# Kernel optimization log

Hardware: AMD Instinct MI355X
Metric: run time of the kernel (lower is better)

Reference implementation:

```python
import jax, jax.numpy as jnp
import numpy as np

B, M, E, K = 2048, 768, 16384, 32
EPS = 1e-8  # torch F.cosine_similarity default eps


def setup_inputs() -> dict:
    key = jax.random.key(0)
    ks = jax.random.split(key, 13)
    s_m = 1.0 / np.sqrt(M)  # nn.Linear(M, E) init bound
    s_e = 1.0 / np.sqrt(E)  # nn.Linear(E, M) init bound
    u = lambda k, shape, s: jax.random.uniform(k, shape, jnp.float32, -s, s)
    return {
        "x": jax.random.normal(ks[0], (B, M), jnp.float32),
        "enc_w": u(ks[1], (E, M), s_m), "enc_b": u(ks[2], (E,), s_m),
        "dec_w": u(ks[3], (M, E), s_e), "dec_b": u(ks[4], (M,), s_e),
        "enc1_w": u(ks[5], (E, M), s_m), "enc1_b": u(ks[6], (E,), s_m),
        "dec1_w": u(ks[7], (M, E), s_e), "dec1_b": u(ks[8], (M,), s_e),
        "enc2_w": u(ks[9], (E, M), s_m), "enc2_b": u(ks[10], (E,), s_m),
        "dec2_w": u(ks[11], (M, E), s_e), "dec2_b": u(ks[12], (M,), s_e),
        "k": K,
    }


def _aux_loss(a_BE, win_BE, c1_BE, c2_BE, dp_ME, d1_ME, d2_ME):
    # Faithful reduction of the B x M x E cosine-similarity along M:
    #   scaled_parent[b,:,e] = dp[:,e]*a[b,e];  scaled_child uses d1/d2 per winner mask.
    # cos_sim needs only M-dim dot products / norms of decoder columns.
    np2_E = jnp.sum(dp_ME * dp_ME, axis=0)   # ||dp_e||^2
    n1_E = jnp.sum(d1_ME * d1_ME, axis=0)
    n2_E = jnp.sum(d2_ME * d2_ME, axis=0)
    dp1_E = jnp.sum(dp_ME * d1_ME, axis=0)   # <dp_e, d1_e>
    dp2_E = jnp.sum(dp_ME * d2_ME, axis=0)
    c_BE = jnp.where(win_BE, c1_BE, c2_BE)
    dpc_BE = jnp.where(win_BE, dp1_E, dp2_E)
    nc_BE = jnp.where(win_BE, n1_E, n2_E)
    a2 = a_BE * a_BE
    dot = a2 * np2_E + a_BE * c_BE * dpc_BE                      # <parent, parent+child>
    norm_p = jnp.abs(a_BE) * jnp.sqrt(np2_E)                     # ||parent||
    comb2 = a2 * np2_E + 2.0 * a_BE * c_BE * dpc_BE + c_BE * c_BE * nc_BE
    norm_c = jnp.sqrt(jnp.maximum(comb2, 0.0))                   # ||parent+child||
    cos = dot / (jnp.maximum(norm_p, EPS) * jnp.maximum(norm_c, EPS))
    active = a_BE > 0
    return -jnp.sum(jnp.where(active, cos, 0.0)) / a_BE.shape[0]


def reference(x, enc_w, enc_b, dec_w, dec_b, enc1_w, enc1_b, dec1_w, dec1_b,
              enc2_w, enc2_b, dec2_w, dec2_b, k):
    Bn = x.shape[0]
    En = enc_w.shape[0]
    pre_BE = x @ enc_w.T + enc_b
    vals, idx = jax.lax.top_k(pre_BE, k)                         # [B,k]
    sae_BE = jnp.zeros_like(pre_BE).at[jnp.arange(Bn)[:, None], idx].set(vals)
    num_live_parent = jnp.zeros((En,), bool).at[idx.ravel()].set(True).sum()

    pre1_BE = x @ enc1_w.T + enc1_b
    pre2_BE = x @ enc2_w.T + enc2_b
    active = sae_BE != 0.0
    m1_BE = jnp.where(active, pre1_BE, 0.0)
    m2_BE = jnp.where(active, pre2_BE, 0.0)
    win_BE = m1_BE > m2_BE
    f1_BE = jnp.where(win_BE, m1_BE, 0.0)
    f2_BE = jnp.where(~win_BE, m2_BE, 0.0)
    num_live_c1 = jnp.any(f1_BE != 0, axis=0).sum()
    num_live_c2 = jnp.any(f2_BE != 0, axis=0).sum()

    recon_BM = (sae_BE @ dec_w.T + dec_b) + (f1_BE @ dec1_w.T + dec1_b) + (f2_BE @ dec2_w.T + dec2_b)

    sg = jax.lax.stop_gradient
    aux = _aux_loss(sg(sae_BE), sg(win_BE), sg(f1_BE), sg(f2_BE), dec_w, dec1_w, dec2_w)
    return recon_BM, (num_live_parent, num_live_c1, num_live_c2), aux
```

## Files before the change

### kernel.cpp

```cpp
#include <hip/hip_runtime.h>
#include <cstdint>
#include <cstddef>

#define B_N 2048
#define M_N 768
#define E_N 16384
#define K_N 32
#define EPSF 1e-8f

typedef __attribute__((ext_vector_type(8))) short short8;
typedef __attribute__((ext_vector_type(4))) float floatx4;
typedef __attribute__((ext_vector_type(4))) unsigned short ushort4v;

__device__ inline unsigned short f2bf(float f) {
  unsigned int u = __float_as_uint(f);
  unsigned int r = (u + 0x7fffu + ((u >> 16) & 1u)) >> 16;
  return (unsigned short)r;
}
__device__ inline float bf2f(unsigned short h) {
  return __uint_as_float(((unsigned int)h) << 16);
}

__global__ __launch_bounds__(256) void split_kernel(const float* __restrict__ in,
                                                    unsigned short* __restrict__ hi,
                                                    unsigned short* __restrict__ lo,
                                                    int n4) {
  int i = blockIdx.x * 256 + threadIdx.x;
  if (i >= n4) return;
  float4 v = ((const float4*)in)[i];
  ushort4v h, l;
  h.x = f2bf(v.x); l.x = f2bf(v.x - bf2f(h.x));
  h.y = f2bf(v.y); l.y = f2bf(v.y - bf2f(h.y));
  h.z = f2bf(v.z); l.z = f2bf(v.z - bf2f(h.z));
  h.w = f2bf(v.w); l.w = f2bf(v.w - bf2f(h.w));
  ((ushort4v*)hi)[i] = h;
  ((ushort4v*)lo)[i] = l;
}

__global__ void prep_dec_kernel(const float* __restrict__ dw, const float* __restrict__ d1,
                                const float* __restrict__ d2,
                                float* __restrict__ dT0, float* __restrict__ dT1,
                                float* __restrict__ dT2, float* __restrict__ stats) {
  __shared__ float t0[32][33], t1[32][33], t2[32][33];
  __shared__ float ps[5][8][32];
  int tx = threadIdx.x;
  int ty = threadIdx.y;
  int e = blockIdx.x * 32 + tx;
  float s0 = 0.f, s1 = 0.f, s2 = 0.f, s3 = 0.f, s4 = 0.f;
  for (int r = 0; r < 32; r += 8) {
    int m = blockIdx.y * 32 + ty + r;
    float a  = dw[(size_t)m * E_N + e];
    float b1 = d1[(size_t)m * E_N + e];
    float b2 = d2[(size_t)m * E_N + e];
    t0[ty + r][tx] = a;
    t1[ty + r][tx] = b1;
    t2[ty + r][tx] = b2;
    s0 = fmaf(a, a, s0);
    s1 = fmaf(b1, b1, s1);
    s2 = fmaf(b2, b2, s2);
    s3 = fmaf(a, b1, s3);
    s4 = fmaf(a, b2, s4);
  }
  ps[0][ty][tx] = s0; ps[1][ty][tx] = s1; ps[2][ty][tx] = s2;
  ps[3][ty][tx] = s3; ps[4][ty][tx] = s4;
  __syncthreads();
  int m2 = blockIdx.y * 32 + tx;
  for (int r = 0; r < 32; r += 8) {
    int e2 = blockIdx.x * 32 + ty + r;
    dT0[(size_t)e2 * M_N + m2] = t0[tx][ty + r];
    dT1[(size_t)e2 * M_N + m2] = t1[tx][ty + r];
    dT2[(size_t)e2 * M_N + m2] = t2[tx][ty + r];
  }
  if (ty == 0) {
    float a0 = 0.f, a1 = 0.f, a2 = 0.f, a3 = 0.f, a4 = 0.f;
#pragma unroll
    for (int q = 0; q < 8; ++q) {
      a0 += ps[0][q][tx]; a1 += ps[1][q][tx]; a2 += ps[2][q][tx];
      a3 += ps[3][q][tx]; a4 += ps[4][q][tx];
    }
    atomicAdd(&stats[e], a0);
    atomicAdd(&stats[E_N + e], a1);
    atomicAdd(&stats[2 * E_N + e], a2);
    atomicAdd(&stats[3 * E_N + e], a3);
    atomicAdd(&stats[4 * E_N + e], a4);
  }
}

#define TM 128
#define TN 128
#define TK 32
#define LDK 40

__global__ __launch_bounds__(256) void gemm_mfma_kernel(
    const unsigned short* __restrict__ Ahi, const unsigned short* __restrict__ Alo,
    const unsigned short* __restrict__ Bhi, const unsigned short* __restrict__ Blo,
    const float* __restrict__ bias, float* __restrict__ C) {
  __shared__ __align__(16) unsigned short As_hi[TM * LDK];
  __shared__ __align__(16) unsigned short As_lo[TM * LDK];
  __shared__ __align__(16) unsigned short Bs_hi[TM * LDK];
  __shared__ __align__(16) unsigned short Bs_lo[TM * LDK];

  int tid = threadIdx.x;
  int lane = tid & 63;
  int wave = tid >> 6;
  int i0 = blockIdx.y * TM;
  int j0 = blockIdx.x * TN;
  int wm = (wave >> 1) * 64;
  int wn = (wave & 1) * 64;

  int row0 = tid >> 2, c40 = tid & 3;
  int row1 = 64 + (tid >> 2), c41 = tid & 3;
  const unsigned short* pAhi0 = Ahi + (size_t)(i0 + row0) * M_N + c40 * 8;
  const unsigned short* pAhi1 = Ahi + (size_t)(i0 + row1) * M_N + c41 * 8;
  const unsigned short* pAlo0 = Alo + (size_t)(i0 + row0) * M_N + c40 * 8;
  const unsigned short* pAlo1 = Alo + (size_t)(i0 + row1) * M_N + c41 * 8;
  const unsigned short* pBhi0 = Bhi + (size_t)(j0 + row0) * M_N + c40 * 8;
  const unsigned short* pBhi1 = Bhi + (size_t)(j0 + row1) * M_N + c41 * 8;
  const unsigned short* pBlo0 = Blo + (size_t)(j0 + row0) * M_N + c40 * 8;
  const unsigned short* pBlo1 = Blo + (size_t)(j0 + row1) * M_N + c41 * 8;
  int l0 = row0 * LDK + c40 * 8;
  int l1 = row1 * LDK + c41 * 8;

  floatx4 acc[4][4];
#pragma unroll
  for (int i = 0; i < 4; ++i)
#pragma unroll
    for (int j = 0; j < 4; ++j) acc[i][j] = (floatx4){0.f, 0.f, 0.f, 0.f};

  int fr = lane & 15;
  int fk = (lane >> 4) * 8;

  short8 vAh0 = *(const short8*)pAhi0;
  short8 vAh1 = *(const short8*)pAhi1;
  short8 vAl0 = *(const short8*)pAlo0;
  short8 vAl1 = *(const short8*)pAlo1;
  short8 vBh0 = *(const short8*)pBhi0;
  short8 vBh1 = *(const short8*)pBhi1;
  short8 vBl0 = *(const short8*)pBlo0;
  short8 vBl1 = *(const short8*)pBlo1;

  for (int k0 = 0; k0 < M_N; k0 += TK) {
    __syncthreads();
    *(short8*)&As_hi[l0] = vAh0;
    *(short8*)&As_hi[l1] = vAh1;
    *(short8*)&As_lo[l0] = vAl0;
    *(short8*)&As_lo[l1] = vAl1;
    *(short8*)&Bs_hi[l0] = vBh0;
    *(short8*)&Bs_hi[l1] = vBh1;
    *(short8*)&Bs_lo[l0] = vBl0;
    *(short8*)&Bs_lo[l1] = vBl1;
    __syncthreads();

    if (k0 + TK < M_N) {
      int d = k0 + TK;
      vAh0 = *(const short8*)(pAhi0 + d);
      vAh1 = *(const short8*)(pAhi1 + d);
      vAl0 = *(const short8*)(pAlo0 + d);
      vAl1 = *(const short8*)(pAlo1 + d);
      vBh0 = *(const short8*)(pBhi0 + d);
      vBh1 = *(const short8*)(pBhi1 + d);
      vBl0 = *(const short8*)(pBlo0 + d);
      vBl1 = *(const short8*)(pBlo1 + d);
    }

    short8 ah[4], al[4], bh[4], bl[4];
#pragma unroll
    for (int t = 0; t < 4; ++t) {
      int ar = (wm + t * 16 + fr) * LDK + fk;
      int br = (wn + t * 16 + fr) * LDK + fk;
      ah[t] = *(const short8*)&As_hi[ar];
      al[t] = *(const short8*)&As_lo[ar];
      bh[t] = *(const short8*)&Bs_hi[br];
      bl[t] = *(const short8*)&Bs_lo[br];
    }
#pragma unroll
    for (int mi = 0; mi < 4; ++mi)
#pragma unroll
      for (int ni = 0; ni < 4; ++ni) {
        acc[mi][ni] = __builtin_amdgcn_mfma_f32_16x16x32_bf16(ah[mi], bh[ni], acc[mi][ni], 0, 0, 0);
        acc[mi][ni] = __builtin_amdgcn_mfma_f32_16x16x32_bf16(ah[mi], bl[ni], acc[mi][ni], 0, 0, 0);
        acc[mi][ni] = __builtin_amdgcn_mfma_f32_16x16x32_bf16(al[mi], bh[ni], acc[mi][ni], 0, 0, 0);
      }
  }

#pragma unroll
  for (int mi = 0; mi < 4; ++mi) {
    int rbase = i0 + wm + mi * 16 + (lane >> 4) * 4;
#pragma unroll
    for (int ni = 0; ni < 4; ++ni) {
      int col = j0 + wn + ni * 16 + (lane & 15);
      float bb = bias[col];
#pragma unroll
      for (int r = 0; r < 4; ++r) {
        C[(size_t)(rbase + r) * E_N + col] = acc[mi][ni][r] + bb;
      }
    }
  }
}

__global__ __launch_bounds__(256) void topk_kernel(const float* __restrict__ pre,
                                                   int* __restrict__ topk_idx,
                                                   float* __restrict__ topk_val,
                                                   int* __restrict__ live_p) {
  int b = blockIdx.x;
  int tid = threadIdx.x;
  const float* row = pre + (size_t)b * E_N;

  __shared__ unsigned int hist[2048];
  __shared__ float candV[2048];
  __shared__ int candI[2048];
  __shared__ float defV[K_N];
  __shared__ int defI[K_N];
  __shared__ int s_T, s_nDef, s_nCand;

  for (int i = tid; i < 2048; i += 256) hist[i] = 0;
  if (tid == 0) { s_nDef = 0; s_nCand = 0; }
  __syncthreads();

  for (int j = 0; j < E_N / 1024; ++j) {
    float4 v = ((const float4*)row)[tid + j * 256];
    float f[4] = {v.x, v.y, v.z, v.w};
#pragma unroll
    for (int q = 0; q < 4; ++q) {
      unsigned int u = __float_as_uint(f[q]);
      unsigned int key = (u & 0x80000000u) ? ~u : (u | 0x80000000u);
      atomicAdd(&hist[key >> 21], 1u);
    }
  }
  __syncthreads();

  if (tid == 0) {
    unsigned int cum = 0;
    for (int bk = 2047; bk >= 0; --bk) {
      cum += hist[bk];
      if (cum >= K_N) { s_T = bk; break; }
    }
  }
  __syncthreads();
  int T = s_T;

  for (int j = 0; j < E_N / 1024; ++j) {
    int i4 = tid + j * 256;
    float4 v = ((const float4*)row)[i4];
    float f[4] = {v.x, v.y, v.z, v.w};
#pragma unroll
    for (int q = 0; q < 4; ++q) {
      float vv = f[q];
      unsigned int u = __float_as_uint(vv);
      unsigned int key = (u & 0x80000000u) ? ~u : (u | 0x80000000u);
      int bk = key >> 21;
      if (bk > T) {
        int d = atomicAdd(&s_nDef, 1);
        defV[d] = vv;
        defI[d] = i4 * 4 + q;
      } else if (bk == T) {
        int c = atomicAdd(&s_nCand, 1);
        candV[c] = vv;
        candI[c] = i4 * 4 + q;
      }
    }
  }
  __syncthreads();
  int nDef = s_nDef;
  int nCand = s_nCand;
  int need = K_N - nDef;

  if (tid < nDef) {
    topk_idx[b * K_N + tid] = defI[tid];
    topk_val[b * K_N + tid] = defV[tid];
    live_p[defI[tid]] = 1;
  }
  for (int c = tid; c < nCand; c += 256) {
    float v = candV[c];
    int idx = candI[c];
    int r = 0;
    for (int j2 = 0; j2 < nCand; ++j2) {
      float vj = candV[j2];
      r += (vj > v) || (vj == v && candI[j2] < idx);
    }
    if (r < need) {
      int slot = nDef + r;
      topk_idx[b * K_N + slot] = idx;
      topk_val[b * K_N + slot] = v;
      live_p[idx] = 1;
    }
  }
}

__global__ __launch_bounds__(256) void child_recon_kernel(
    const float* __restrict__ x, const float* __restrict__ e1w, const float* __restrict__ e1b,
    const float* __restrict__ e2w, const float* __restrict__ e2b,
    const int* __restrict__ topk_idx, const float* __restrict__ topk_val,
    int* __restrict__ live_c1, int* __restrict__ live_c2,
    const float* __restrict__ stats, float* __restrict__ aux_sum,
    const float* __restrict__ decT0, const float* __restrict__ decT1,
    const float* __restrict__ decT2,
    const float* __restrict__ db0, const float* __restrict__ db1,
    const float* __restrict__ db2, float* __restrict__ out) {
  int b = blockIdx.x;
  int tid = threadIdx.x;
  int lane = tid & 63;
  int wave = tid >> 6;

  __shared__ float xs[M_N];
  __shared__ int es[K_N];
  __shared__ float as[K_N], cs[K_N];
  __shared__ int wf[K_N];
  __shared__ float wsum[4];

  if (tid < K_N) {
    es[tid] = topk_idx[b * K_N + tid];
    as[tid] = topk_val[b * K_N + tid];
  }
  for (int i = tid; i < M_N; i += 256) xs[i] = x[(size_t)b * M_N + i];
  __syncthreads();

  float cos_acc = 0.f;
  for (int s = wave; s < K_N; s += 4) {
    int e = es[s];
    float a = as[s];
    if (a != 0.f) {
      float d1 = 0.f, d2 = 0.f;
#pragma unroll
      for (int j = 0; j < 3; ++j) {
        int m = (lane << 2) + j * 256;
        float4 xv = *(const float4*)&xs[m];
        float4 w1 = *(const float4*)&e1w[(size_t)e * M_N + m];
        float4 w2 = *(const float4*)&e2w[(size_t)e * M_N + m];
        d1 += xv.x * w1.x + xv.y * w1.y + xv.z * w1.z + xv.w * w1.w;
        d2 += xv.x * w2.x + xv.y * w2.y + xv.z * w2.z + xv.w * w2.w;
      }
#pragma unroll
      for (int off = 32; off > 0; off >>= 1) {
        d1 += __shfl_down(d1, off);
        d2 += __shfl_down(d2, off);
      }
      if (lane == 0) {
        float m1 = d1 + e1b[e];
        float m2 = d2 + e2b[e];
        bool win = m1 > m2;
        float f1 = win ? m1 : 0.f;
        float f2 = win ? 0.f : m2;
        float c = win ? f1 : f2;
        cs[s] = c;
        wf[s] = win ? 1 : 0;
        if (f1 != 0.f) live_c1[e] = 1;
        if (f2 != 0.f) live_c2[e] = 1;
        if (a > 0.f) {
          float np2e = stats[e];
          float nce = win ? stats[E_N + e] : stats[2 * E_N + e];
          float dpc = win ? stats[3 * E_N + e] : stats[4 * E_N + e];
          float a2 = a * a;
          float dot = a2 * np2e + a * c * dpc;
          float normp = fabsf(a) * sqrtf(np2e);
          float comb2 = a2 * np2e + 2.f * a * c * dpc + c * c * nce;
          float normc = sqrtf(fmaxf(comb2, 0.f));
          cos_acc += dot / (fmaxf(normp, EPSF) * fmaxf(normc, EPSF));
        }
      }
    } else if (lane == 0) {
      cs[s] = 0.f;
      wf[s] = 0;
    }
  }
  if (lane == 0) wsum[wave] = cos_acc;
  __syncthreads();
  if (tid == 0) atomicAdd(aux_sum, wsum[0] + wsum[1] + wsum[2] + wsum[3]);

  float acc0 = db0[tid] + db1[tid] + db2[tid];
  float acc1 = db0[tid + 256] + db1[tid + 256] + db2[tid + 256];
  float acc2 = db0[tid + 512] + db1[tid + 512] + db2[tid + 512];

  for (int s = 0; s < K_N; ++s) {
    float a = as[s];
    float c = cs[s];
    if (a == 0.f && c == 0.f) continue;
    int e = es[s];
    const float* col = decT0 + (size_t)e * M_N;
    acc0 = fmaf(a, col[tid], acc0);
    acc1 = fmaf(a, col[tid + 256], acc1);
    acc2 = fmaf(a, col[tid + 512], acc2);
    if (c != 0.f) {
      const float* ccol = (wf[s] ? decT1 : decT2) + (size_t)e * M_N;
      acc0 = fmaf(c, ccol[tid], acc0);
      acc1 = fmaf(c, ccol[tid + 256], acc1);
      acc2 = fmaf(c, ccol[tid + 512], acc2);
    }
  }
  out[(size_t)b * M_N + tid] = acc0;
  out[(size_t)b * M_N + tid + 256] = acc1;
  out[(size_t)b * M_N + tid + 512] = acc2;
}

__global__ void finalize_kernel(const int* __restrict__ live_p, const int* __restrict__ live_c1,
                                const int* __restrict__ live_c2, const float* __restrict__ aux_sum,
                                float* __restrict__ out_tail) {
  int tid = threadIdx.x;
  int c0 = 0, c1 = 0, c2 = 0;
  for (int i = tid; i < E_N; i += 256) {
    c0 += live_p[i];
    c1 += live_c1[i];
    c2 += live_c2[i];
  }
  __shared__ int r0[256], r1[256], r2[256];
  r0[tid] = c0; r1[tid] = c1; r2[tid] = c2;
  __syncthreads();
  for (int s = 128; s > 0; s >>= 1) {
    if (tid < s) { r0[tid] += r0[tid + s]; r1[tid] += r1[tid + s]; r2[tid] += r2[tid + s]; }
    __syncthreads();
  }
  if (tid == 0) {
    out_tail[0] = (float)r0[0];
    out_tail[1] = (float)r1[0];
    out_tail[2] = (float)r2[0];
    out_tail[3] = -aux_sum[0] / (float)B_N;
  }
}

extern "C" void kernel_launch(void* const* d_in, const int* in_sizes, int n_in,
                              void* d_out, int out_size, void* d_ws, size_t ws_size,
                              hipStream_t stream) {
  const float* x     = (const float*)d_in[0];
  const float* enc_w = (const float*)d_in[1];
  const float* enc_b = (const float*)d_in[2];
  const float* dec_w = (const float*)d_in[3];
  const float* dec_b = (const float*)d_in[4];
  const float* e1w   = (const float*)d_in[5];
  const float* e1b   = (const float*)d_in[6];
  const float* d1w   = (const float*)d_in[7];
  const float* d1b   = (const float*)d_in[8];
  const float* e2w   = (const float*)d_in[9];
  const float* e2b   = (const float*)d_in[10];
  const float* d2w   = (const float*)d_in[11];
  const float* d2b   = (const float*)d_in[12];

  float* wsf = (float*)d_ws;

  const size_t PRE_F = (size_t)B_N * E_N;
  const size_t XSP_F = (size_t)B_N * M_N / 2;
  const size_t ESP_F = (size_t)E_N * M_N / 2;
  const size_t DEC_F = (size_t)E_N * M_N;
  const size_t BIG_F = PRE_F + 2 * XSP_F + 2 * ESP_F;

  float* pre = wsf;
  unsigned short* xhi  = (unsigned short*)(wsf + PRE_F);
  unsigned short* xlo  = (unsigned short*)(wsf + PRE_F + XSP_F);
  unsigned short* ewhi = (unsigned short*)(wsf + PRE_F + 2 * XSP_F);
  unsigned short* ewlo = (unsigned short*)(wsf + PRE_F + 2 * XSP_F + ESP_F);
  float* decT0 = wsf;
  float* decT1 = wsf + DEC_F;
  float* decT2 = wsf + 2 * DEC_F;

  size_t off = BIG_F;
  float* stats  = wsf + off;
  int*   livep  = (int*)(wsf + off + 5 * (size_t)E_N);
  int*   livec1 = livep + E_N;
  int*   livec2 = livep + 2 * E_N;
  float* auxs   = (float*)(livep + 3 * E_N);
  off += 8 * (size_t)E_N + 64;
  off &= ~(size_t)63;
  int*   tidx = (int*)(wsf + off);    off += (size_t)B_N * K_N;
  float* tval = wsf + off;            off += (size_t)B_N * K_N;

  hipMemsetAsync(stats, 0, (8 * (size_t)E_N + 1) * sizeof(float), stream);

  split_kernel<<<(B_N * M_N / 4 + 255) / 256, 256, 0, stream>>>(x, xhi, xlo, B_N * M_N / 4);
  split_kernel<<<(E_N * M_N / 4 + 255) / 256, 256, 0, stream>>>(enc_w, ewhi, ewlo, E_N * M_N / 4);

  gemm_mfma_kernel<<<dim3(E_N / TN, B_N / TM), 256, 0, stream>>>(xhi, xlo, ewhi, ewlo, enc_b, pre);

  topk_kernel<<<B_N, 256, 0, stream>>>(pre, tidx, tval, livep);

  prep_dec_kernel<<<dim3(E_N / 32, M_N / 32), dim3(32, 8), 0, stream>>>(
      dec_w, d1w, d2w, decT0, decT1, decT2, stats);

  float* out = (float*)d_out;
  child_recon_kernel<<<B_N, 256, 0, stream>>>(x, e1w, e1b, e2w, e2b, tidx, tval,
                                              livec1, livec2, stats, auxs,
                                              decT0, decT1, decT2, dec_b, d1b, d2b, out);

  finalize_kernel<<<1, 256, 0, stream>>>(livep, livec1, livec2, auxs,
                                         out + (size_t)B_N * M_N);
}
```

Before: 691.0 us.

## Merge split kernels, parallelize top-k threshold scan, split encoder GEMM in halves

Merges the two bf16 hi/lo split launches into one kernel. In top-k, the shared histogram becomes four per-wave copies to reduce atomic contention, and the serial single-thread threshold search is replaced by a block-wide suffix scan. The encoder GEMM is launched as two half-batch kernels on the same stream. That split gives no overlap by itself and adds a launch, while the extra histogram copies increase LDS use.

```diff
diff --git a/kernel.cpp b/kernel.cpp
--- a/kernel.cpp
+++ b/kernel.cpp
@@ -21,20 +21,31 @@
   return __uint_as_float(((unsigned int)h) << 16);
 }
 
-__global__ __launch_bounds__(256) void split_kernel(const float* __restrict__ in,
-                                                    unsigned short* __restrict__ hi,
-                                                    unsigned short* __restrict__ lo,
-                                                    int n4) {
+__global__ __launch_bounds__(256) void split2_kernel(
+    const float* __restrict__ inA, unsigned short* __restrict__ hiA,
+    unsigned short* __restrict__ loA, int n4A,
+    const float* __restrict__ inB, unsigned short* __restrict__ hiB,
+    unsigned short* __restrict__ loB, int n4B) {
   int i = blockIdx.x * 256 + threadIdx.x;
-  if (i >= n4) return;
-  float4 v = ((const float4*)in)[i];
+  const float* in;
+  unsigned short* hi;
+  unsigned short* lo;
+  int idx;
+  if (i < n4A) {
+    in = inA; hi = hiA; lo = loA; idx = i;
+  } else {
+    idx = i - n4A;
+    if (idx >= n4B) return;
+    in = inB; hi = hiB; lo = loB;
+  }
+  float4 v = ((const float4*)in)[idx];
   ushort4v h, l;
   h.x = f2bf(v.x); l.x = f2bf(v.x - bf2f(h.x));
   h.y = f2bf(v.y); l.y = f2bf(v.y - bf2f(h.y));
   h.z = f2bf(v.z); l.z = f2bf(v.z - bf2f(h.z));
   h.w = f2bf(v.w); l.w = f2bf(v.w - bf2f(h.w));
-  ((ushort4v*)hi)[i] = h;
-  ((ushort4v*)lo)[i] = l;
+  ((ushort4v*)hi)[idx] = h;
+  ((ushort4v*)lo)[idx] = l;
 }
 
 __global__ void prep_dec_kernel(const float* __restrict__ dw, const float* __restrict__ d1,
@@ -204,16 +215,20 @@
                                                    int* __restrict__ live_p) {
   int b = blockIdx.x;
   int tid = threadIdx.x;
+  int wave = tid >> 6;
   const float* row = pre + (size_t)b * E_N;
 
-  __shared__ unsigned int hist[2048];
+  __shared__ __align__(16) unsigned int hist4[4][2048];
+  __shared__ unsigned int csum[256];
   __shared__ float candV[2048];
   __shared__ int candI[2048];
   __shared__ float defV[K_N];
   __shared__ int defI[K_N];
   __shared__ int s_T, s_nDef, s_nCand;
 
-  for (int i = tid; i < 2048; i += 256) hist[i] = 0;
+  uint4 z4 = make_uint4(0u, 0u, 0u, 0u);
+  uint4* hz = (uint4*)&hist4[0][0];
+  for (int i = tid; i < 2048; i += 256) hz[i] = z4;
   if (tid == 0) { s_nDef = 0; s_nCand = 0; }
   __syncthreads();
 
@@ -224,16 +239,41 @@
     for (int q = 0; q < 4; ++q) {
       unsigned int u = __float_as_uint(f[q]);
       unsigned int key = (u & 0x80000000u) ? ~u : (u | 0x80000000u);
-      atomicAdd(&hist[key >> 21], 1u);
-    }
-  }
-  __syncthreads();
-
-  if (tid == 0) {
-    unsigned int cum = 0;
-    for (int bk = 2047; bk >= 0; --bk) {
-      cum += hist[bk];
-      if (cum >= K_N) { s_T = bk; break; }
+      atomicAdd(&hist4[wave][key >> 21], 1u);
+    }
+  }
+  __syncthreads();
+
+  unsigned int hm[8];
+#pragma unroll
+  for (int i = 0; i < 8; ++i) hm[i] = 0u;
+#pragma unroll
+  for (int w = 0; w < 4; ++w) {
+    uint4 p0 = *(const uint4*)&hist4[w][tid * 8];
+    uint4 p1 = *(const uint4*)&hist4[w][tid * 8 + 4];
+    hm[0] += p0.x; hm[1] += p0.y; hm[2] += p0.z; hm[3] += p0.w;
+    hm[4] += p1.x; hm[5] += p1.y; hm[6] += p1.z; hm[7] += p1.w;
+  }
+  unsigned int sc = hm[0] + hm[1] + hm[2] + hm[3] + hm[4] + hm[5] + hm[6] + hm[7];
+  csum[tid] = sc;
+  __syncthreads();
+  for (int off = 1; off < 256; off <<= 1) {
+    unsigned int v_ = (tid + off < 256) ? csum[tid + off] : 0u;
+    __syncthreads();
+    csum[tid] += v_;
+    __syncthreads();
+  }
+  {
+    unsigned int above = (tid < 255) ? csum[tid + 1] : 0u;
+    if (csum[tid] >= K_N && above < K_N) {
+      unsigned int run = above;
+      int T = 0;
+#pragma unroll
+      for (int i = 7; i >= 0; --i) {
+        run += hm[i];
+        if (run >= K_N) { T = tid * 8 + i; break; }
+      }
+      s_T = T;
     }
   }
   __syncthreads();
@@ -464,10 +504,16 @@
 
   hipMemsetAsync(stats, 0, (8 * (size_t)E_N + 1) * sizeof(float), stream);
 
-  split_kernel<<<(B_N * M_N / 4 + 255) / 256, 256, 0, stream>>>(x, xhi, xlo, B_N * M_N / 4);
-  split_kernel<<<(E_N * M_N / 4 + 255) / 256, 256, 0, stream>>>(enc_w, ewhi, ewlo, E_N * M_N / 4);
-
-  gemm_mfma_kernel<<<dim3(E_N / TN, B_N / TM), 256, 0, stream>>>(xhi, xlo, ewhi, ewlo, enc_b, pre);
+  int n4A = B_N * M_N / 4;
+  int n4B = E_N * M_N / 4;
+  split2_kernel<<<(n4A + n4B + 255) / 256, 256, 0, stream>>>(x, xhi, xlo, n4A,
+                                                             enc_w, ewhi, ewlo, n4B);
+
+  const int HB = B_N / 2;
+  gemm_mfma_kernel<<<dim3(E_N / TN, HB / TM), 256, 0, stream>>>(xhi, xlo, ewhi, ewlo, enc_b, pre);
+  gemm_mfma_kernel<<<dim3(E_N / TN, HB / TM), 256, 0, stream>>>(
+      xhi + (size_t)HB * M_N, xlo + (size_t)HB * M_N, ewhi, ewlo, enc_b,
+      pre + (size_t)HB * E_N);
 
   topk_kernel<<<B_N, 256, 0, stream>>>(pre, tidx, tval, livep);
 
```

After: 662.5 us. -4.1%, faster.
